# Kernel optimization log

Measured on AMD Instinct MI355X. Metric: run time of the kernel, lower is better.

Reference implementation:

```python
import jax, jax.numpy as jnp
import numpy as np

D_MODEL = 1024
MAX_LEN = 2048
BATCH = 4


def _causal_mask(max_len):
    # tril ones -> 0 on/below diag, -inf above (added to scores BEFORE scaling,
    # matching the original module's order of operations)
    return jnp.where(jnp.tril(jnp.ones((max_len, max_len), dtype=bool)), 0.0, -jnp.inf).astype(jnp.float32)


def setup_inputs() -> dict:
    key = jax.random.key(0)
    ks = jax.random.split(key, 9)
    s = 1.0 / np.sqrt(D_MODEL)  # torch Linear default init scale (uniform bound)
    return {
        "encoded_q": jax.random.normal(ks[0], (BATCH, MAX_LEN, D_MODEL), jnp.float32),
        "encoded_k": jax.random.normal(ks[1], (BATCH, MAX_LEN, D_MODEL), jnp.float32),
        "encoded_v": jax.random.normal(ks[2], (BATCH, MAX_LEN, D_MODEL), jnp.float32),
        "W_q": jax.random.uniform(ks[3], (D_MODEL, D_MODEL), jnp.float32, -s, s),
        "b_q": jax.random.uniform(ks[4], (D_MODEL,), jnp.float32, -s, s),
        "W_k": jax.random.uniform(ks[5], (D_MODEL, D_MODEL), jnp.float32, -s, s),
        "b_k": jax.random.uniform(ks[6], (D_MODEL,), jnp.float32, -s, s),
        "W_v": jax.random.uniform(ks[7], (D_MODEL, D_MODEL), jnp.float32, -s, s),
        "b_v": jax.random.uniform(ks[8], (D_MODEL,), jnp.float32, -s, s),
        "parameter_mask": 1,
    }


def reference(encoded_q, encoded_k, encoded_v, W_q, b_q, W_k, b_k, W_v, b_v, parameter_mask):
    # torch Linear: y = x @ W.T + b
    q = jnp.einsum("bsd,ed->bse", encoded_q, W_q) + b_q  # [B,S,D]
    k = jnp.einsum("bsd,ed->bse", encoded_k, W_k) + b_k
    v = jnp.einsum("bsd,ed->bse", encoded_v, W_v) + b_v
    values = jnp.einsum("bqd,bkd->bqk", q, k)  # [B,S,S]
    if parameter_mask:
        values = values + _causal_mask(values.shape[-1])
    scaled = values / jnp.sqrt(jnp.float32(D_MODEL))
    attn = jax.nn.softmax(scaled, axis=-1)
    return jnp.einsum("bqk,bkd->bqd", attn, v)  # [B,S,D]
```

## Files before the change

### kernel.cpp

```cpp
#include <hip/hip_runtime.h>

typedef __bf16 bf16;
typedef __attribute__((ext_vector_type(8))) __bf16 bf16x8;
typedef __attribute__((ext_vector_type(4))) __bf16 bf16x4;
typedef __attribute__((ext_vector_type(4))) float f32x4;

#define S_LEN 2048
#define DM 1024
#define NB 4

__device__ __forceinline__ void async_copy16(const void* g, void* l)
{
    __builtin_amdgcn_global_load_lds(
        (const __attribute__((address_space(1))) unsigned int*)g,
        (__attribute__((address_space(3))) unsigned int*)l,
        16, 0, 0);
}

__device__ __forceinline__ void gemm_tile(
    const bf16* __restrict__ A, int lda,
    const bf16* __restrict__ B, int ldb,
    int kSteps, bf16* sA, bf16* sB, f32x4 (&acc)[4][4])
{
    const int tid = threadIdx.x;
    const int w = tid >> 6, lane = tid & 63;
    const int quad = lane >> 4, l16 = lane & 15;
    const int wr = w >> 1, wc = w & 1;

#pragma unroll
    for (int i = 0; i < 4; i++)
#pragma unroll
        for (int j = 0; j < 4; j++) acc[i][j] = f32x4{0.f, 0.f, 0.f, 0.f};

    const int srow = tid >> 3;
    const int sc8  = tid & 7;
    const int srcCol = (sc8 ^ (srow & 7)) * 16;
    const char* aG = (const char*)(A + (size_t)srow * lda) + srcCol;
    const char* bG = (const char*)(B + (size_t)srow * ldb) + srcCol;
    char* aL = (char*)sA + w * 1024;
    char* bL = (char*)sB + w * 1024;
    const size_t aRow32 = (size_t)lda * 64;
    const size_t bRow32 = (size_t)ldb * 64;

    const int swz = l16 & 7;

    for (int ks = 0; ks < kSteps; ks++) {
        const char* aGk = aG + (size_t)ks * 128;
        const char* bGk = bG + (size_t)ks * 128;
#pragma unroll
        for (int i = 0; i < 4; i++) {
            async_copy16(aGk + i * aRow32, aL + i * 4096);
            async_copy16(bGk + i * bRow32, bL + i * 4096);
        }
        __syncthreads();
#pragma unroll
        for (int kk = 0; kk < 2; kk++) {
            bf16x8 af[4], bfr[4];
#pragma unroll
            for (int t = 0; t < 4; t++) {
                const int ca = ((kk * 4 + quad) ^ swz) * 16;
                af[t]  = *(const bf16x8*)((const char*)sA + (wr * 64 + t * 16 + l16) * 128 + ca);
                bfr[t] = *(const bf16x8*)((const char*)sB + (wc * 64 + t * 16 + l16) * 128 + ca);
            }
#pragma unroll
            for (int rt = 0; rt < 4; rt++)
#pragma unroll
                for (int ct = 0; ct < 4; ct++)
                    acc[rt][ct] = __builtin_amdgcn_mfma_f32_16x16x32_bf16(
                        af[rt], bfr[ct], acc[rt][ct], 0, 0, 0);
        }
        __syncthreads();
    }
}

__global__ __launch_bounds__(256) void cvt3_kernel(
    const float* __restrict__ s0, const float* __restrict__ s1, const float* __restrict__ s2,
    bf16* __restrict__ d0, bf16* __restrict__ d1, bf16* __restrict__ d2)
{
    const float* src = blockIdx.y == 0 ? s0 : blockIdx.y == 1 ? s1 : s2;
    bf16* dst        = blockIdx.y == 0 ? d0 : blockIdx.y == 1 ? d1 : d2;
    size_t i = ((size_t)blockIdx.x * 256 + threadIdx.x) * 8;
    f32x4 a = *(const f32x4*)(src + i);
    f32x4 b = *(const f32x4*)(src + i + 4);
    bf16x8 o;
    o[0] = (bf16)a[0]; o[1] = (bf16)a[1]; o[2] = (bf16)a[2]; o[3] = (bf16)a[3];
    o[4] = (bf16)b[0]; o[5] = (bf16)b[1]; o[6] = (bf16)b[2]; o[7] = (bf16)b[3];
    *(bf16x8*)(dst + i) = o;
}

__global__ __launch_bounds__(256) void proj_kernel(
    const bf16* __restrict__ Eq, const bf16* __restrict__ Ek, const bf16* __restrict__ Ev,
    const bf16* __restrict__ Wq, const bf16* __restrict__ Wk, const bf16* __restrict__ Wv,
    const float* __restrict__ bq, const float* __restrict__ bk, const float* __restrict__ bv,
    bf16* __restrict__ Qo, bf16* __restrict__ Ko, bf16* __restrict__ Vt)
{
    __shared__ __align__(16) bf16 sA[128 * 64];
    __shared__ __align__(16) bf16 sB[128 * 64];
    const int z = blockIdx.z;
    const bf16* E     = z == 0 ? Eq : z == 1 ? Ek : Ev;
    const bf16* W     = z == 0 ? Wq : z == 1 ? Wk : Wv;
    const float* bias = z == 0 ? bq : z == 1 ? bk : bv;
    const int n0 = blockIdx.x * 128;
    const int m0 = blockIdx.y * 128;

    f32x4 acc[4][4];
    gemm_tile(E + (size_t)m0 * DM, DM, W + (size_t)n0 * DM, DM, DM / 64, sA, sB, acc);

    const int tid = threadIdx.x;
    const int w = tid >> 6, lane = tid & 63;
    const int quad = lane >> 4, l16 = lane & 15;
    const int wr = w >> 1, wc = w & 1;
    const int mBase = m0 + wr * 64;
    const int nBase = n0 + wc * 64;

    float bcol[4];
#pragma unroll
    for (int ct = 0; ct < 4; ct++) bcol[ct] = bias[nBase + ct * 16 + l16];

    if (z < 2) {
        bf16* O = z == 0 ? Qo : Ko;
#pragma unroll
        for (int rt = 0; rt < 4; rt++)
#pragma unroll
            for (int ct = 0; ct < 4; ct++)
#pragma unroll
                for (int r = 0; r < 4; r++) {
                    const int m = mBase + rt * 16 + quad * 4 + r;
                    const int n = nBase + ct * 16 + l16;
                    O[(size_t)m * DM + n] = (bf16)(acc[rt][ct][r] + bcol[ct]);
                }
    } else {
#pragma unroll
        for (int rt = 0; rt < 4; rt++) {
            const int m = mBase + rt * 16 + quad * 4;
            const int bb = m >> 11;
            const int s  = m & 2047;
#pragma unroll
            for (int ct = 0; ct < 4; ct++) {
                const int n = nBase + ct * 16 + l16;
                bf16x4 o;
                o[0] = (bf16)(acc[rt][ct][0] + bcol[ct]);
                o[1] = (bf16)(acc[rt][ct][1] + bcol[ct]);
                o[2] = (bf16)(acc[rt][ct][2] + bcol[ct]);
                o[3] = (bf16)(acc[rt][ct][3] + bcol[ct]);
                *(bf16x4*)(Vt + ((size_t)(bb * DM + n)) * S_LEN + s) = o;
            }
        }
    }
}

__global__ __launch_bounds__(256) void qk_kernel(
    const bf16* __restrict__ Q, const bf16* __restrict__ K,
    const int* __restrict__ maskp, bf16* __restrict__ P, float* __restrict__ lsum)
{
    const int b = blockIdx.y;
    const bool causal = (maskp[0] != 0);
    const int nQt = S_LEN / 128;
    const int nCausal = nQt * (nQt + 1) / 2;
    int qt, kt;
    if (causal) {
        const int t = blockIdx.x;
        if (t >= nCausal) return;
        qt = (int)((__fsqrt_rn(8.0f * t + 1.0f) - 1.0f) * 0.5f);
        while ((qt + 1) * (qt + 2) / 2 <= t) qt++;
        while (qt * (qt + 1) / 2 > t) qt--;
        kt = t - qt * (qt + 1) / 2;
    } else {
        qt = blockIdx.x >> 4;
        kt = blockIdx.x & 15;
    }

    __shared__ __align__(16) bf16 sA[128 * 64];
    __shared__ __align__(16) bf16 sB[128 * 64];

    f32x4 acc[4][4];
    const bf16* Qb = Q + ((size_t)(b * S_LEN + qt * 128)) * DM;
    const bf16* Kb = K + ((size_t)(b * S_LEN + kt * 128)) * DM;
    gemm_tile(Qb, DM, Kb, DM, DM / 64, sA, sB, acc);

    const int tid = threadIdx.x;
    const int w = tid >> 6, lane = tid & 63;
    const int quad = lane >> 4, l16 = lane & 15;
    const int wr = w >> 1, wc = w & 1;
    const float scale = 0.03125f;

    bf16* Pb = P + (size_t)b * S_LEN * S_LEN;
    float* lb = lsum + b * S_LEN;

#pragma unroll
    for (int rt = 0; rt < 4; rt++)
#pragma unroll
        for (int r = 0; r < 4; r++) {
            const int qg = qt * 128 + wr * 64 + rt * 16 + quad * 4 + r;
            float rs = 0.0f;
#pragma unroll
            for (int ct = 0; ct < 4; ct++) {
                const int kg = kt * 128 + wc * 64 + ct * 16 + l16;
                float p = (!causal || kg <= qg) ? __expf(acc[rt][ct][r] * scale) : 0.0f;
                bf16 pb = (bf16)p;
                Pb[(size_t)qg * S_LEN + kg] = pb;
                rs += (float)pb;
            }
#pragma unroll
            for (int off = 1; off < 16; off <<= 1) rs += __shfl_xor(rs, off);
            if (l16 == 0) atomicAdd(&lb[qg], rs);
        }
}

__global__ __launch_bounds__(256) void pv_kernel(
    const bf16* __restrict__ P, const bf16* __restrict__ Vt,
    const float* __restrict__ lsum, const int* __restrict__ maskp,
    float* __restrict__ Out)
{
    const int dt = blockIdx.x, b = blockIdx.z;
    const int qt = (S_LEN / 128 - 1) - blockIdx.y;
    const bool causal = (maskp[0] != 0);
    const int kSteps = causal ? (qt + 1) * 2 : (S_LEN / 64);

    __shared__ __align__(16) bf16 sA[128 * 64];
    __shared__ __align__(16) bf16 sB[128 * 64];

    f32x4 acc[4][4];
    const bf16* Pb = P + ((size_t)b * S_LEN + qt * 128) * S_LEN;
    const bf16* Vb = Vt + ((size_t)(b * DM + dt * 128)) * S_LEN;
    gemm_tile(Pb, S_LEN, Vb, S_LEN, kSteps, sA, sB, acc);

    const int tid = threadIdx.x;
    const int w = tid >> 6, lane = tid & 63;
    const int quad = lane >> 4, l16 = lane & 15;
    const int wr = w >> 1, wc = w & 1;

    const float* lb = lsum + b * S_LEN;
#pragma unroll
    for (int rt = 0; rt < 4; rt++)
#pragma unroll
        for (int r = 0; r < 4; r++) {
            const int qg = qt * 128 + wr * 64 + rt * 16 + quad * 4 + r;
            const float inv = 1.0f / lb[qg];
#pragma unroll
            for (int ct = 0; ct < 4; ct++) {
                const int dg = dt * 128 + wc * 64 + ct * 16 + l16;
                Out[((size_t)(b * S_LEN + qg)) * DM + dg] = acc[rt][ct][r] * inv;
            }
        }
}

extern "C" void kernel_launch(void* const* d_in, const int* in_sizes, int n_in,
                              void* d_out, int out_size, void* d_ws, size_t ws_size,
                              hipStream_t stream)
{
    const float* Eq = (const float*)d_in[0];
    const float* Ek = (const float*)d_in[1];
    const float* Ev = (const float*)d_in[2];
    const float* Wq = (const float*)d_in[3];
    const float* bq = (const float*)d_in[4];
    const float* Wk = (const float*)d_in[5];
    const float* bk = (const float*)d_in[6];
    const float* Wv = (const float*)d_in[7];
    const float* bv = (const float*)d_in[8];
    const int* maskp = (const int*)d_in[9];
    float* Out = (float*)d_out;

    char* ws = (char*)d_ws;
    const size_t SZ_QKV = (size_t)NB * S_LEN * DM * 2;
    const size_t SZ_W   = (size_t)DM * DM * 2;
    bf16* Qb  = (bf16*)(ws);
    bf16* Kb  = (bf16*)(ws + SZ_QKV);
    bf16* Vtb = (bf16*)(ws + 2 * SZ_QKV);
    bf16* Wqb = (bf16*)(ws + 3 * SZ_QKV);
    bf16* Wkb = (bf16*)(ws + 3 * SZ_QKV + SZ_W);
    bf16* Wvb = (bf16*)(ws + 3 * SZ_QKV + 2 * SZ_W);
    float* lsum = (float*)(ws + 3 * SZ_QKV + 3 * SZ_W);
    bf16* Pbuf = (bf16*)(ws + 3 * SZ_QKV + 3 * SZ_W + (1 << 20));
    bf16* Eqb = Pbuf;
    bf16* Ekb = Eqb + (size_t)NB * S_LEN * DM;
    bf16* Evb = Ekb + (size_t)NB * S_LEN * DM;

    cvt3_kernel<<<dim3(512, 3), 256, 0, stream>>>(Wq, Wk, Wv, Wqb, Wkb, Wvb);
    cvt3_kernel<<<dim3(4096, 3), 256, 0, stream>>>(Eq, Ek, Ev, Eqb, Ekb, Evb);

    proj_kernel<<<dim3(DM / 128, NB * S_LEN / 128, 3), 256, 0, stream>>>(
        Eqb, Ekb, Evb, Wqb, Wkb, Wvb, bq, bk, bv, Qb, Kb, Vtb);

    hipMemsetAsync(lsum, 0, (size_t)NB * S_LEN * 4, stream);

    qk_kernel<<<dim3(256, NB), 256, 0, stream>>>(Qb, Kb, maskp, Pbuf, lsum);
    pv_kernel<<<dim3(DM / 128, S_LEN / 128, NB), 256, 0, stream>>>(Pbuf, Vtb, lsum, maskp, Out);
}
```

Baseline: 317.4 us.

## Stage GEMM epilogues through LDS for coalesced stores and remap block indices

The Q/K projection, the P tile and the output epilogues now write accumulators into a padded LDS tile first, then issue wide coalesced 16-byte global stores. The old path did scattered 2- or 4-byte per-lane stores. Row sums in qk are now computed from the staged tile, with one atomic per row pair instead of per 16-lane group. Grids are flattened to 1D with a remapping so that consecutive blocks (mod 8) group tiles sharing operands, likely for XCD/L2 locality, and causal qk pairs light and heavy tiles. This adds extra LDS traffic and barriers, and qk now launches blocks that exit early for masked tiles.

```diff
diff --git a/kernel.cpp b/kernel.cpp
--- a/kernel.cpp
+++ b/kernel.cpp
@@ -20,8 +20,10 @@
 __device__ __forceinline__ void gemm_tile(
     const bf16* __restrict__ A, int lda,
     const bf16* __restrict__ B, int ldb,
-    int kSteps, bf16* sA, bf16* sB, f32x4 (&acc)[4][4])
-{
+    int kSteps, char* smem, f32x4 (&acc)[4][4])
+{
+    bf16* sA = (bf16*)smem;
+    bf16* sB = (bf16*)(smem + 16384);
     const int tid = threadIdx.x;
     const int w = tid >> 6, lane = tid & 63;
     const int quad = lane >> 4, l16 = lane & 15;
@@ -94,23 +96,27 @@
     const float* __restrict__ bq, const float* __restrict__ bk, const float* __restrict__ bv,
     bf16* __restrict__ Qo, bf16* __restrict__ Ko, bf16* __restrict__ Vt)
 {
-    __shared__ __align__(16) bf16 sA[128 * 64];
-    __shared__ __align__(16) bf16 sB[128 * 64];
-    const int z = blockIdx.z;
+    __shared__ __align__(16) char smem[34816];
+    const int bid = blockIdx.x;
+    const int c = bid & 7;
+    const int j = bid >> 3;
+    const int z = j >> 6;
+    const int r64 = j & 63;
+    const int mTile = c * 8 + (r64 >> 3);
+    const int nTile = r64 & 7;
+    const int m0 = mTile * 128, n0 = nTile * 128;
+
     const bf16* E     = z == 0 ? Eq : z == 1 ? Ek : Ev;
     const bf16* W     = z == 0 ? Wq : z == 1 ? Wk : Wv;
     const float* bias = z == 0 ? bq : z == 1 ? bk : bv;
-    const int n0 = blockIdx.x * 128;
-    const int m0 = blockIdx.y * 128;
 
     f32x4 acc[4][4];
-    gemm_tile(E + (size_t)m0 * DM, DM, W + (size_t)n0 * DM, DM, DM / 64, sA, sB, acc);
+    gemm_tile(E + (size_t)m0 * DM, DM, W + (size_t)n0 * DM, DM, DM / 64, smem, acc);
 
     const int tid = threadIdx.x;
     const int w = tid >> 6, lane = tid & 63;
     const int quad = lane >> 4, l16 = lane & 15;
     const int wr = w >> 1, wc = w & 1;
-    const int mBase = m0 + wr * 64;
     const int nBase = n0 + wc * 64;
 
     float bcol[4];
@@ -118,18 +124,25 @@
     for (int ct = 0; ct < 4; ct++) bcol[ct] = bias[nBase + ct * 16 + l16];
 
     if (z < 2) {
+        bf16* Tt = (bf16*)smem;
+#pragma unroll
+        for (int rt = 0; rt < 4; rt++)
+#pragma unroll
+            for (int ct = 0; ct < 4; ct++)
+#pragma unroll
+                for (int r = 0; r < 4; r++)
+                    Tt[(wr * 64 + rt * 16 + quad * 4 + r) * 136 + wc * 64 + ct * 16 + l16]
+                        = (bf16)(acc[rt][ct][r] + bcol[ct]);
+        __syncthreads();
         bf16* O = z == 0 ? Qo : Ko;
-#pragma unroll
-        for (int rt = 0; rt < 4; rt++)
-#pragma unroll
-            for (int ct = 0; ct < 4; ct++)
-#pragma unroll
-                for (int r = 0; r < 4; r++) {
-                    const int m = mBase + rt * 16 + quad * 4 + r;
-                    const int n = nBase + ct * 16 + l16;
-                    O[(size_t)m * DM + n] = (bf16)(acc[rt][ct][r] + bcol[ct]);
-                }
+        const int row = tid >> 1, half = tid & 1;
+        const bf16* src = Tt + row * 136 + half * 64;
+        bf16* dst = O + (size_t)(m0 + row) * DM + n0 + half * 64;
+#pragma unroll
+        for (int i = 0; i < 8; i++)
+            *(bf16x8*)(dst + i * 8) = *(const bf16x8*)(src + i * 8);
     } else {
+        const int mBase = m0 + wr * 64;
 #pragma unroll
         for (int rt = 0; rt < 4; rt++) {
             const int m = mBase + rt * 16 + quad * 4;
@@ -153,30 +166,22 @@
     const bf16* __restrict__ Q, const bf16* __restrict__ K,
     const int* __restrict__ maskp, bf16* __restrict__ P, float* __restrict__ lsum)
 {
-    const int b = blockIdx.y;
+    const int bid = blockIdx.x;
+    const int c = bid & 7;
+    const int j = bid >> 3;
+    const int b = j >> 5;
+    const int jj = j & 31;
+    const int kt = (jj < 16) ? c : (15 - c);
+    const int qt = jj & 15;
     const bool causal = (maskp[0] != 0);
-    const int nQt = S_LEN / 128;
-    const int nCausal = nQt * (nQt + 1) / 2;
-    int qt, kt;
-    if (causal) {
-        const int t = blockIdx.x;
-        if (t >= nCausal) return;
-        qt = (int)((__fsqrt_rn(8.0f * t + 1.0f) - 1.0f) * 0.5f);
-        while ((qt + 1) * (qt + 2) / 2 <= t) qt++;
-        while (qt * (qt + 1) / 2 > t) qt--;
-        kt = t - qt * (qt + 1) / 2;
-    } else {
-        qt = blockIdx.x >> 4;
-        kt = blockIdx.x & 15;
-    }
-
-    __shared__ __align__(16) bf16 sA[128 * 64];
-    __shared__ __align__(16) bf16 sB[128 * 64];
+    if (causal && kt > qt) return;
+
+    __shared__ __align__(16) char smem[34816];
 
     f32x4 acc[4][4];
     const bf16* Qb = Q + ((size_t)(b * S_LEN + qt * 128)) * DM;
     const bf16* Kb = K + ((size_t)(b * S_LEN + kt * 128)) * DM;
-    gemm_tile(Qb, DM, Kb, DM, DM / 64, sA, sB, acc);
+    gemm_tile(Qb, DM, Kb, DM, DM / 64, smem, acc);
 
     const int tid = threadIdx.x;
     const int w = tid >> 6, lane = tid & 63;
@@ -184,27 +189,37 @@
     const int wr = w >> 1, wc = w & 1;
     const float scale = 0.03125f;
 
-    bf16* Pb = P + (size_t)b * S_LEN * S_LEN;
-    float* lb = lsum + b * S_LEN;
-
+    bf16* Pt = (bf16*)smem;
 #pragma unroll
     for (int rt = 0; rt < 4; rt++)
 #pragma unroll
         for (int r = 0; r < 4; r++) {
-            const int qg = qt * 128 + wr * 64 + rt * 16 + quad * 4 + r;
-            float rs = 0.0f;
+            const int rloc = wr * 64 + rt * 16 + quad * 4 + r;
+            const int qg = qt * 128 + rloc;
 #pragma unroll
             for (int ct = 0; ct < 4; ct++) {
                 const int kg = kt * 128 + wc * 64 + ct * 16 + l16;
                 float p = (!causal || kg <= qg) ? __expf(acc[rt][ct][r] * scale) : 0.0f;
-                bf16 pb = (bf16)p;
-                Pb[(size_t)qg * S_LEN + kg] = pb;
-                rs += (float)pb;
+                Pt[rloc * 136 + wc * 64 + ct * 16 + l16] = (bf16)p;
             }
-#pragma unroll
-            for (int off = 1; off < 16; off <<= 1) rs += __shfl_xor(rs, off);
-            if (l16 == 0) atomicAdd(&lb[qg], rs);
-        }
+        }
+    __syncthreads();
+
+    bf16* Pb = P + (size_t)b * S_LEN * S_LEN;
+    float* lb = lsum + b * S_LEN;
+    const int row = tid >> 1, half = tid & 1;
+    const bf16* src = Pt + row * 136 + half * 64;
+    bf16* dst = Pb + (size_t)(qt * 128 + row) * S_LEN + kt * 128 + half * 64;
+    float rs = 0.0f;
+#pragma unroll
+    for (int i = 0; i < 8; i++) {
+        bf16x8 x = *(const bf16x8*)(src + i * 8);
+        *(bf16x8*)(dst + i * 8) = x;
+#pragma unroll
+        for (int e = 0; e < 8; e++) rs += (float)x[e];
+    }
+    rs += __shfl_xor(rs, 1);
+    if (half == 0) atomicAdd(&lb[qt * 128 + row], rs);
 }
 
 __global__ __launch_bounds__(256) void pv_kernel(
@@ -212,18 +227,20 @@
     const float* __restrict__ lsum, const int* __restrict__ maskp,
     float* __restrict__ Out)
 {
-    const int dt = blockIdx.x, b = blockIdx.z;
-    const int qt = (S_LEN / 128 - 1) - blockIdx.y;
+    const int bid = blockIdx.x;
+    const int dt = bid & 7;
+    const int j = bid >> 3;
+    const int b = j >> 4;
+    const int qt = 15 - (j & 15);
     const bool causal = (maskp[0] != 0);
     const int kSteps = causal ? (qt + 1) * 2 : (S_LEN / 64);
 
-    __shared__ __align__(16) bf16 sA[128 * 64];
-    __shared__ __align__(16) bf16 sB[128 * 64];
+    __shared__ __align__(16) char smem[33792];
 
     f32x4 acc[4][4];
     const bf16* Pb = P + ((size_t)b * S_LEN + qt * 128) * S_LEN;
     const bf16* Vb = Vt + ((size_t)(b * DM + dt * 128)) * S_LEN;
-    gemm_tile(Pb, S_LEN, Vb, S_LEN, kSteps, sA, sB, acc);
+    gemm_tile(Pb, S_LEN, Vb, S_LEN, kSteps, smem, acc);
 
     const int tid = threadIdx.x;
     const int w = tid >> 6, lane = tid & 63;
@@ -231,18 +248,36 @@
     const int wr = w >> 1, wc = w & 1;
 
     const float* lb = lsum + b * S_LEN;
+    float inv[4][4];
 #pragma unroll
     for (int rt = 0; rt < 4; rt++)
 #pragma unroll
-        for (int r = 0; r < 4; r++) {
-            const int qg = qt * 128 + wr * 64 + rt * 16 + quad * 4 + r;
-            const float inv = 1.0f / lb[qg];
-#pragma unroll
-            for (int ct = 0; ct < 4; ct++) {
-                const int dg = dt * 128 + wc * 64 + ct * 16 + l16;
-                Out[((size_t)(b * S_LEN + qg)) * DM + dg] = acc[rt][ct][r] * inv;
-            }
-        }
+        for (int r = 0; r < 4; r++)
+            inv[rt][r] = 1.0f / lb[qt * 128 + wr * 64 + rt * 16 + quad * 4 + r];
+
+    float* Ot = (float*)smem;
+#pragma unroll
+    for (int h = 0; h < 2; h++) {
+        if (wr == h) {
+#pragma unroll
+            for (int rt = 0; rt < 4; rt++)
+#pragma unroll
+                for (int r = 0; r < 4; r++) {
+                    const int rloc = rt * 16 + quad * 4 + r;
+#pragma unroll
+                    for (int ct = 0; ct < 4; ct++)
+                        Ot[rloc * 132 + wc * 64 + ct * 16 + l16] = acc[rt][ct][r] * inv[rt][r];
+                }
+        }
+        __syncthreads();
+        const int row = tid >> 2, qq = tid & 3;
+        const float* src = Ot + row * 132 + qq * 32;
+        float* dst = Out + (size_t)(b * S_LEN + qt * 128 + h * 64 + row) * DM + dt * 128 + qq * 32;
+#pragma unroll
+        for (int i = 0; i < 8; i++)
+            *(f32x4*)(dst + i * 4) = *(const f32x4*)(src + i * 4);
+        __syncthreads();
+    }
 }
 
 extern "C" void kernel_launch(void* const* d_in, const int* in_sizes, int n_in,
@@ -276,14 +311,13 @@
     bf16* Ekb = Eqb + (size_t)NB * S_LEN * DM;
     bf16* Evb = Ekb + (size_t)NB * S_LEN * DM;
 
+    hipMemsetAsync(lsum, 0, (size_t)NB * S_LEN * 4, stream);
     cvt3_kernel<<<dim3(512, 3), 256, 0, stream>>>(Wq, Wk, Wv, Wqb, Wkb, Wvb);
     cvt3_kernel<<<dim3(4096, 3), 256, 0, stream>>>(Eq, Ek, Ev, Eqb, Ekb, Evb);
 
-    proj_kernel<<<dim3(DM / 128, NB * S_LEN / 128, 3), 256, 0, stream>>>(
+    proj_kernel<<<1536, 256, 0, stream>>>(
         Eqb, Ekb, Evb, Wqb, Wkb, Wvb, bq, bk, bv, Qb, Kb, Vtb);
 
-    hipMemsetAsync(lsum, 0, (size_t)NB * S_LEN * 4, stream);
-
-    qk_kernel<<<dim3(256, NB), 256, 0, stream>>>(Qb, Kb, maskp, Pbuf, lsum);
-    pv_kernel<<<dim3(DM / 128, S_LEN / 128, NB), 256, 0, stream>>>(Pbuf, Vtb, lsum, maskp, Out);
-}
+    qk_kernel<<<1024, 256, 0, stream>>>(Qb, Kb, maskp, Pbuf, lsum);
+    pv_kernel<<<512, 256, 0, stream>>>(Pbuf, Vtb, lsum, maskp, Out);
+}
```

New measurement: 314.3 us. No clear change (-1.0%).

## Switch GEMMs to single-wave 128x64 tiles with double-buffered async LDS pipeline

Applied to the files above, without the earlier changes.

Replaces the 4-wave 128x128 block GEMM with a single-wave 128x64 tile that double-buffers its async global-to-LDS copies and uses vmcnt waits instead of block barriers, so loads overlap MFMA work. Grid indexing is remapped with an XCD-aware interleave (blockIdx & 7) and a causal load-balancing order for QK tiles. Each wave now holds 32 accumulators and a 48KB LDS buffer at one block per CU by launch bounds, which limits occupancy and latency hiding.

```diff
diff --git a/kernel.cpp b/kernel.cpp
--- a/kernel.cpp
+++ b/kernel.cpp
@@ -17,59 +17,86 @@
         16, 0, 0);
 }
 
-__device__ __forceinline__ void gemm_tile(
-    const bf16* __restrict__ A, int lda,
-    const bf16* __restrict__ B, int ldb,
-    int kSteps, bf16* sA, bf16* sB, f32x4 (&acc)[4][4])
-{
-    const int tid = threadIdx.x;
-    const int w = tid >> 6, lane = tid & 63;
+__device__ __forceinline__ void vm_wait24() { asm volatile("s_waitcnt vmcnt(24)" ::: "memory"); }
+__device__ __forceinline__ void vm_wait0()  { asm volatile("s_waitcnt vmcnt(0)"  ::: "memory"); }
+
+
+__device__ __forceinline__ void wave_issue(const char* aG, size_t ldaB,
+                                           const char* bG, size_t ldbB,
+                                           char* buf)
+{
+#pragma unroll
+    for (int i = 0; i < 16; i++)
+        async_copy16(aG + (size_t)i * 8 * ldaB, buf + i * 1024);
+#pragma unroll
+    for (int j = 0; j < 8; j++)
+        async_copy16(bG + (size_t)j * 8 * ldbB, buf + 16384 + j * 1024);
+}
+
+__device__ __forceinline__ void wave_frags(const char* buf, int l16, int quad,
+                                           bf16x8 (&af)[2][8], bf16x8 (&bfr)[2][4])
+{
+    const int swz = l16 & 7;
+#pragma unroll
+    for (int kk = 0; kk < 2; kk++) {
+        const int col = (((kk << 2) + quad) ^ swz) << 4;
+#pragma unroll
+        for (int t = 0; t < 8; t++)
+            af[kk][t] = *(const bf16x8*)(buf + (t * 16 + l16) * 128 + col);
+#pragma unroll
+        for (int t = 0; t < 4; t++)
+            bfr[kk][t] = *(const bf16x8*)(buf + 16384 + (t * 16 + l16) * 128 + col);
+    }
+}
+
+__device__ __forceinline__ void wave_mfma(const bf16x8 (&af)[2][8],
+                                          const bf16x8 (&bfr)[2][4],
+                                          f32x4 (&acc)[8][4])
+{
+#pragma unroll
+    for (int kk = 0; kk < 2; kk++)
+#pragma unroll
+        for (int rt = 0; rt < 8; rt++)
+#pragma unroll
+            for (int ct = 0; ct < 4; ct++)
+                acc[rt][ct] = __builtin_amdgcn_mfma_f32_16x16x32_bf16(
+                    af[kk][rt], bfr[kk][ct], acc[rt][ct], 0, 0, 0);
+}
+
+__device__ __forceinline__ void wave_gemm(const bf16* __restrict__ A, int lda,
+                                          const bf16* __restrict__ B, int ldb,
+                                          int kSteps, char* smem, f32x4 (&acc)[8][4])
+{
+    const int lane = threadIdx.x & 63;
     const int quad = lane >> 4, l16 = lane & 15;
-    const int wr = w >> 1, wc = w & 1;
-
-#pragma unroll
-    for (int i = 0; i < 4; i++)
+    const int r8 = lane >> 3, c8 = lane & 7;
+    const size_t ldaB = (size_t)lda * 2, ldbB = (size_t)ldb * 2;
+    const char* aG = (const char*)A + (size_t)r8 * ldaB + ((c8 ^ r8) << 4);
+    const char* bG = (const char*)B + (size_t)r8 * ldbB + ((c8 ^ r8) << 4);
+
+#pragma unroll
+    for (int i = 0; i < 8; i++)
 #pragma unroll
         for (int j = 0; j < 4; j++) acc[i][j] = f32x4{0.f, 0.f, 0.f, 0.f};
 
-    const int srow = tid >> 3;
-    const int sc8  = tid & 7;
-    const int srcCol = (sc8 ^ (srow & 7)) * 16;
-    const char* aG = (const char*)(A + (size_t)srow * lda) + srcCol;
-    const char* bG = (const char*)(B + (size_t)srow * ldb) + srcCol;
-    char* aL = (char*)sA + w * 1024;
-    char* bL = (char*)sB + w * 1024;
-    const size_t aRow32 = (size_t)lda * 64;
-    const size_t bRow32 = (size_t)ldb * 64;
-
-    const int swz = l16 & 7;
-
-    for (int ks = 0; ks < kSteps; ks++) {
-        const char* aGk = aG + (size_t)ks * 128;
-        const char* bGk = bG + (size_t)ks * 128;
-#pragma unroll
-        for (int i = 0; i < 4; i++) {
-            async_copy16(aGk + i * aRow32, aL + i * 4096);
-            async_copy16(bGk + i * bRow32, bL + i * 4096);
-        }
-        __syncthreads();
-#pragma unroll
-        for (int kk = 0; kk < 2; kk++) {
-            bf16x8 af[4], bfr[4];
-#pragma unroll
-            for (int t = 0; t < 4; t++) {
-                const int ca = ((kk * 4 + quad) ^ swz) * 16;
-                af[t]  = *(const bf16x8*)((const char*)sA + (wr * 64 + t * 16 + l16) * 128 + ca);
-                bfr[t] = *(const bf16x8*)((const char*)sB + (wc * 64 + t * 16 + l16) * 128 + ca);
-            }
-#pragma unroll
-            for (int rt = 0; rt < 4; rt++)
-#pragma unroll
-                for (int ct = 0; ct < 4; ct++)
-                    acc[rt][ct] = __builtin_amdgcn_mfma_f32_16x16x32_bf16(
-                        af[rt], bfr[ct], acc[rt][ct], 0, 0, 0);
-        }
-        __syncthreads();
+    wave_issue(aG, ldaB, bG, ldbB, smem);
+    wave_issue(aG + 128, ldaB, bG + 128, ldbB, smem + 24576);
+
+    for (int ks = 0; ks < kSteps; ks += 2) {
+        bf16x8 af[2][8], bfr[2][4];
+        const bool more = (ks + 2 < kSteps);
+        vm_wait24();
+        wave_frags(smem, l16, quad, af, bfr);
+        if (more)
+            wave_issue(aG + (size_t)(ks + 2) * 128, ldaB,
+                       bG + (size_t)(ks + 2) * 128, ldbB, smem);
+        wave_mfma(af, bfr, acc);
+        if (more) vm_wait24(); else vm_wait0();
+        wave_frags(smem + 24576, l16, quad, af, bfr);
+        if (more)
+            wave_issue(aG + (size_t)(ks + 3) * 128, ldaB,
+                       bG + (size_t)(ks + 3) * 128, ldbB, smem + 24576);
+        wave_mfma(af, bfr, acc);
     }
 }
 
@@ -88,56 +115,55 @@
     *(bf16x8*)(dst + i) = o;
 }
 
-__global__ __launch_bounds__(256) void proj_kernel(
+__global__ __launch_bounds__(64, 1) void proj_kernel(
     const bf16* __restrict__ Eq, const bf16* __restrict__ Ek, const bf16* __restrict__ Ev,
     const bf16* __restrict__ Wq, const bf16* __restrict__ Wk, const bf16* __restrict__ Wv,
     const float* __restrict__ bq, const float* __restrict__ bk, const float* __restrict__ bv,
     bf16* __restrict__ Qo, bf16* __restrict__ Ko, bf16* __restrict__ Vt)
 {
-    __shared__ __align__(16) bf16 sA[128 * 64];
-    __shared__ __align__(16) bf16 sB[128 * 64];
-    const int z = blockIdx.z;
+    __shared__ __align__(16) char smem[49152];
+    const int c = blockIdx.x & 7;
+    const int idx = blockIdx.x >> 3;
+    const int z = idx >> 7;
+    const int r = idx & 127;
+    const int m0 = ((r >> 4) * 8 + c) * 128;
+    const int n0 = (r & 15) * 64;
+
     const bf16* E     = z == 0 ? Eq : z == 1 ? Ek : Ev;
     const bf16* W     = z == 0 ? Wq : z == 1 ? Wk : Wv;
     const float* bias = z == 0 ? bq : z == 1 ? bk : bv;
-    const int n0 = blockIdx.x * 128;
-    const int m0 = blockIdx.y * 128;
-
-    f32x4 acc[4][4];
-    gemm_tile(E + (size_t)m0 * DM, DM, W + (size_t)n0 * DM, DM, DM / 64, sA, sB, acc);
-
-    const int tid = threadIdx.x;
-    const int w = tid >> 6, lane = tid & 63;
+
+    f32x4 acc[8][4];
+    wave_gemm(E + (size_t)m0 * DM, DM, W + (size_t)n0 * DM, DM, DM / 64, smem, acc);
+
+    const int lane = threadIdx.x & 63;
     const int quad = lane >> 4, l16 = lane & 15;
-    const int wr = w >> 1, wc = w & 1;
-    const int mBase = m0 + wr * 64;
-    const int nBase = n0 + wc * 64;
 
     float bcol[4];
 #pragma unroll
-    for (int ct = 0; ct < 4; ct++) bcol[ct] = bias[nBase + ct * 16 + l16];
+    for (int ct = 0; ct < 4; ct++) bcol[ct] = bias[n0 + ct * 16 + l16];
 
     if (z < 2) {
         bf16* O = z == 0 ? Qo : Ko;
 #pragma unroll
-        for (int rt = 0; rt < 4; rt++)
+        for (int rt = 0; rt < 8; rt++)
 #pragma unroll
             for (int ct = 0; ct < 4; ct++)
 #pragma unroll
-                for (int r = 0; r < 4; r++) {
-                    const int m = mBase + rt * 16 + quad * 4 + r;
-                    const int n = nBase + ct * 16 + l16;
-                    O[(size_t)m * DM + n] = (bf16)(acc[rt][ct][r] + bcol[ct]);
+                for (int r2 = 0; r2 < 4; r2++) {
+                    const int m = m0 + rt * 16 + quad * 4 + r2;
+                    const int n = n0 + ct * 16 + l16;
+                    O[(size_t)m * DM + n] = (bf16)(acc[rt][ct][r2] + bcol[ct]);
                 }
     } else {
 #pragma unroll
-        for (int rt = 0; rt < 4; rt++) {
-            const int m = mBase + rt * 16 + quad * 4;
+        for (int rt = 0; rt < 8; rt++) {
+            const int m = m0 + rt * 16 + quad * 4;
             const int bb = m >> 11;
             const int s  = m & 2047;
 #pragma unroll
             for (int ct = 0; ct < 4; ct++) {
-                const int n = nBase + ct * 16 + l16;
+                const int n = n0 + ct * 16 + l16;
                 bf16x4 o;
                 o[0] = (bf16)(acc[rt][ct][0] + bcol[ct]);
                 o[1] = (bf16)(acc[rt][ct][1] + bcol[ct]);
@@ -149,98 +175,89 @@
     }
 }
 
-__global__ __launch_bounds__(256) void qk_kernel(
+__global__ __launch_bounds__(64, 1) void qk_kernel(
     const bf16* __restrict__ Q, const bf16* __restrict__ K,
     const int* __restrict__ maskp, bf16* __restrict__ P, float* __restrict__ lsum)
 {
-    const int b = blockIdx.y;
+    const int c = blockIdx.x & 7;
+    const int idx = blockIdx.x >> 3;
+    const int b = idx >> 6;
+    const int r = idx & 63;
+    const int qt = r >> 2;
+    const int sel = r & 3;
+    const int kt = sel == 0 ? c : sel == 1 ? 31 - c : sel == 2 ? 8 + c : 23 - c;
     const bool causal = (maskp[0] != 0);
-    const int nQt = S_LEN / 128;
-    const int nCausal = nQt * (nQt + 1) / 2;
-    int qt, kt;
-    if (causal) {
-        const int t = blockIdx.x;
-        if (t >= nCausal) return;
-        qt = (int)((__fsqrt_rn(8.0f * t + 1.0f) - 1.0f) * 0.5f);
-        while ((qt + 1) * (qt + 2) / 2 <= t) qt++;
-        while (qt * (qt + 1) / 2 > t) qt--;
-        kt = t - qt * (qt + 1) / 2;
-    } else {
-        qt = blockIdx.x >> 4;
-        kt = blockIdx.x & 15;
-    }
-
-    __shared__ __align__(16) bf16 sA[128 * 64];
-    __shared__ __align__(16) bf16 sB[128 * 64];
-
-    f32x4 acc[4][4];
+    if (causal && kt >= (qt + 1) * 2) return;
+
+    __shared__ __align__(16) char smem[49152];
+    f32x4 acc[8][4];
     const bf16* Qb = Q + ((size_t)(b * S_LEN + qt * 128)) * DM;
-    const bf16* Kb = K + ((size_t)(b * S_LEN + kt * 128)) * DM;
-    gemm_tile(Qb, DM, Kb, DM, DM / 64, sA, sB, acc);
-
-    const int tid = threadIdx.x;
-    const int w = tid >> 6, lane = tid & 63;
+    const bf16* Kb = K + ((size_t)(b * S_LEN + kt * 64)) * DM;
+    wave_gemm(Qb, DM, Kb, DM, DM / 64, smem, acc);
+
+    const int lane = threadIdx.x & 63;
     const int quad = lane >> 4, l16 = lane & 15;
-    const int wr = w >> 1, wc = w & 1;
     const float scale = 0.03125f;
 
     bf16* Pb = P + (size_t)b * S_LEN * S_LEN;
     float* lb = lsum + b * S_LEN;
 
 #pragma unroll
-    for (int rt = 0; rt < 4; rt++)
-#pragma unroll
-        for (int r = 0; r < 4; r++) {
-            const int qg = qt * 128 + wr * 64 + rt * 16 + quad * 4 + r;
+    for (int rt = 0; rt < 8; rt++)
+#pragma unroll
+        for (int r2 = 0; r2 < 4; r2++) {
+            const int qg = qt * 128 + rt * 16 + quad * 4 + r2;
             float rs = 0.0f;
 #pragma unroll
             for (int ct = 0; ct < 4; ct++) {
-                const int kg = kt * 128 + wc * 64 + ct * 16 + l16;
-                float p = (!causal || kg <= qg) ? __expf(acc[rt][ct][r] * scale) : 0.0f;
+                const int kg = kt * 64 + ct * 16 + l16;
+                float p = (!causal || kg <= qg) ? __expf(acc[rt][ct][r2] * scale) : 0.0f;
                 bf16 pb = (bf16)p;
                 Pb[(size_t)qg * S_LEN + kg] = pb;
                 rs += (float)pb;
             }
-#pragma unroll
-            for (int off = 1; off < 16; off <<= 1) rs += __shfl_xor(rs, off);
+            rs += __shfl_xor(rs, 1);
+            rs += __shfl_xor(rs, 2);
+            rs += __shfl_xor(rs, 4);
+            rs += __shfl_xor(rs, 8);
             if (l16 == 0) atomicAdd(&lb[qg], rs);
         }
 }
 
-__global__ __launch_bounds__(256) void pv_kernel(
+__global__ __launch_bounds__(64, 1) void pv_kernel(
     const bf16* __restrict__ P, const bf16* __restrict__ Vt,
     const float* __restrict__ lsum, const int* __restrict__ maskp,
     float* __restrict__ Out)
 {
-    const int dt = blockIdx.x, b = blockIdx.z;
-    const int qt = (S_LEN / 128 - 1) - blockIdx.y;
+    const int c = blockIdx.x & 7;
+    const int idx = blockIdx.x >> 3;
+    const int b = idx >> 5;
+    const int r = idx & 31;
+    const int qt = 15 - (r >> 1);
+    const int dt = (r & 1) * 8 + c;
     const bool causal = (maskp[0] != 0);
     const int kSteps = causal ? (qt + 1) * 2 : (S_LEN / 64);
 
-    __shared__ __align__(16) bf16 sA[128 * 64];
-    __shared__ __align__(16) bf16 sB[128 * 64];
-
-    f32x4 acc[4][4];
+    __shared__ __align__(16) char smem[49152];
+    f32x4 acc[8][4];
     const bf16* Pb = P + ((size_t)b * S_LEN + qt * 128) * S_LEN;
-    const bf16* Vb = Vt + ((size_t)(b * DM + dt * 128)) * S_LEN;
-    gemm_tile(Pb, S_LEN, Vb, S_LEN, kSteps, sA, sB, acc);
-
-    const int tid = threadIdx.x;
-    const int w = tid >> 6, lane = tid & 63;
+    const bf16* Vb = Vt + ((size_t)(b * DM + dt * 64)) * S_LEN;
+    wave_gemm(Pb, S_LEN, Vb, S_LEN, kSteps, smem, acc);
+
+    const int lane = threadIdx.x & 63;
     const int quad = lane >> 4, l16 = lane & 15;
-    const int wr = w >> 1, wc = w & 1;
-
     const float* lb = lsum + b * S_LEN;
-#pragma unroll
-    for (int rt = 0; rt < 4; rt++)
-#pragma unroll
-        for (int r = 0; r < 4; r++) {
-            const int qg = qt * 128 + wr * 64 + rt * 16 + quad * 4 + r;
+
+#pragma unroll
+    for (int rt = 0; rt < 8; rt++)
+#pragma unroll
+        for (int r2 = 0; r2 < 4; r2++) {
+            const int qg = qt * 128 + rt * 16 + quad * 4 + r2;
             const float inv = 1.0f / lb[qg];
 #pragma unroll
             for (int ct = 0; ct < 4; ct++) {
-                const int dg = dt * 128 + wc * 64 + ct * 16 + l16;
-                Out[((size_t)(b * S_LEN + qg)) * DM + dg] = acc[rt][ct][r] * inv;
+                const int dg = dt * 64 + ct * 16 + l16;
+                Out[((size_t)(b * S_LEN + qg)) * DM + dg] = acc[rt][ct][r2] * inv;
             }
         }
 }
@@ -276,14 +293,13 @@
     bf16* Ekb = Eqb + (size_t)NB * S_LEN * DM;
     bf16* Evb = Ekb + (size_t)NB * S_LEN * DM;
 
+    hipMemsetAsync(lsum, 0, (size_t)NB * S_LEN * 4, stream);
     cvt3_kernel<<<dim3(512, 3), 256, 0, stream>>>(Wq, Wk, Wv, Wqb, Wkb, Wvb);
     cvt3_kernel<<<dim3(4096, 3), 256, 0, stream>>>(Eq, Ek, Ev, Eqb, Ekb, Evb);
 
-    proj_kernel<<<dim3(DM / 128, NB * S_LEN / 128, 3), 256, 0, stream>>>(
+    proj_kernel<<<3072, 64, 0, stream>>>(
         Eqb, Ekb, Evb, Wqb, Wkb, Wvb, bq, bk, bv, Qb, Kb, Vtb);
 
-    hipMemsetAsync(lsum, 0, (size_t)NB * S_LEN * 4, stream);
-
-    qk_kernel<<<dim3(256, NB), 256, 0, stream>>>(Qb, Kb, maskp, Pbuf, lsum);
-    pv_kernel<<<dim3(DM / 128, S_LEN / 128, NB), 256, 0, stream>>>(Pbuf, Vtb, lsum, maskp, Out);
-}
+    qk_kernel<<<2048, 64, 0, stream>>>(Qb, Kb, maskp, Pbuf, lsum);
+    pv_kernel<<<1024, 64, 0, stream>>>(Pbuf, Vtb, lsum, maskp, Out);
+}
```

Measured after the change: 347.9 us. +9.6%, slower.
